# Performance work log

Measured on AMD Instinct MI355X. Metric: run time of the kernel, lower is better.

Reference implementation:

```python
import jax, jax.numpy as jnp
import numpy as np

B, H, S, D = 2, 12, 2048, 64

def setup_inputs() -> dict:
    key = jax.random.key(0)
    kq, kk, kv = jax.random.split(key, 3)
    Q = jax.random.normal(kq, (B, H, S, D), dtype=jnp.float32)
    K = jax.random.normal(kk, (B, H, S, D), dtype=jnp.float32)
    V = jax.random.normal(kv, (B, H, S, D), dtype=jnp.float32)
    return {"Q": Q, "K": K, "V": V}

def reference(Q, K, V):
    # NOTE: original code scales by sqrt(Q.shape[-2]) (the sequence length),
    # not the head dim — reproduced faithfully.
    scale = 1.0 / np.sqrt(Q.shape[-2]).astype(np.float32)
    scores = jnp.einsum('bhqd,bhkd->bhqk', Q, K) * scale  # [B,H,S,S]
    attn = jax.nn.softmax(scores, axis=-1)
    context = jnp.einsum('bhqk,bhkd->bhqd', attn, V)      # [B,H,S,D]
    # torch .squeeze(-1) only removes the last dim if it is size 1; D=64 so no-op
    return context
```

## Files before the change

### kernel.cpp

```cpp
#include <hip/hip_runtime.h>
#include <hip/hip_bf16.h>
#include <math.h>
#include <stdint.h>

#define BATCH 2
#define NH 12
#define SEQ 2048
#define HD 64
#define TQ 64
#define TK 64
#define NHEADS (BATCH*NH)
#define NIT (SEQ / TK)

typedef short bf16x8 __attribute__((ext_vector_type(8)));
typedef float f32x4 __attribute__((ext_vector_type(4)));
typedef float f32x16 __attribute__((ext_vector_type(16)));
typedef unsigned short us4_t __attribute__((ext_vector_type(4)));
typedef unsigned short us8_t __attribute__((ext_vector_type(8)));
typedef unsigned int u32x4 __attribute__((ext_vector_type(4)));

#if __has_builtin(__builtin_amdgcn_exp2f)
#define EXP2F(x) __builtin_amdgcn_exp2f(x)
#else
#define EXP2F(x) exp2f(x)
#endif

static __device__ __forceinline__ unsigned short f2bf(float f) {
    unsigned int u = __float_as_uint(f);
    u += 0x7fffu + ((u >> 16) & 1u);
    return (unsigned short)(u >> 16);
}

static __device__ __forceinline__ unsigned int pack2bf(float a, float b) {
    __hip_bfloat162 v = __float22bfloat162_rn(float2{a, b});
    return *(unsigned int*)&v;
}

static __device__ __forceinline__ void async_cp16(const void* g, void* l) {
    __builtin_amdgcn_global_load_lds(
        (const __attribute__((address_space(1))) void*)g,
        (__attribute__((address_space(3))) void*)(uintptr_t)l,
        16, 0, 0);
}

static __device__ __forceinline__ int tile_off(int r, int c) {
    int rp  = r >> 1;
    int pos = (((r & 1) << 3) | c) ^ (rp & 15);
    return rp * 128 + pos * 8;
}

__global__ __launch_bounds__(256)
void prep_kv(const float* __restrict__ K, const float* __restrict__ V,
             unsigned short* __restrict__ Kb, unsigned short* __restrict__ Vtb) {
    __shared__ unsigned short T[64][66];
    const int bh = blockIdx.x >> 5;
    const int s0 = (blockIdx.x & 31) * 64;
    const int tid = threadIdx.x;
    const size_t off = ((size_t)bh * SEQ + s0) * HD;

    #pragma unroll
    for (int u = 0; u < 4; ++u) {
        int idx = u * 1024 + tid * 4;
        float4 a = *(const float4*)&K[off + idx];
        us4_t r4 = { f2bf(a.x), f2bf(a.y), f2bf(a.z), f2bf(a.w) };
        *(us4_t*)&Kb[off + idx] = r4;
    }
    #pragma unroll
    for (int u = 0; u < 4; ++u) {
        int idx = u * 1024 + tid * 4;
        int r = idx >> 6, col = idx & 63;
        float4 a = *(const float4*)&V[off + idx];
        *(unsigned int*)&T[r][col]     = pack2bf(a.x, a.y);
        *(unsigned int*)&T[r][col + 2] = pack2bf(a.z, a.w);
    }
    __syncthreads();
    unsigned short* Vdst = Vtb + (size_t)bh * HD * SEQ;
    const int g = tid & 7, dd = tid >> 3;
    #pragma unroll
    for (int h = 0; h < 2; ++h) {
        int d = dd + 32 * h;
        us8_t r8;
        #pragma unroll
        for (int j = 0; j < 8; ++j) {
            int src = ((g >> 1) << 4) + ((j >> 2) << 3) + ((g & 1) << 2) + (j & 3);
            r8[j] = T[src][d];
        }
        *(us8_t*)&Vdst[(size_t)d * SEQ + s0 + g * 8] = r8;
    }
}

__global__ __launch_bounds__(256, 4)
void fa_main(const float* __restrict__ Q,
             const unsigned short* __restrict__ Kb,
             const unsigned short* __restrict__ Vtb,
             float* __restrict__ O, float qs) {
    const int x  = blockIdx.x & 7;
    const int t  = blockIdx.x >> 3;
    const int bh = x + 8 * (t % 3);
    const int qt = t / 3;
    const int q0 = qt * TQ;

    __shared__ __align__(16) unsigned char SH[33280];
    unsigned short* Ksh0 = (unsigned short*)SH;
    unsigned short* Ksh1 = (unsigned short*)(SH + 8192);
    unsigned short* Vsh0 = (unsigned short*)(SH + 16384);
    unsigned short* Vsh1 = (unsigned short*)(SH + 24576);
    float* Lsum = (float*)(SH + 32768);
    float* Linv = (float*)(SH + 33024);
    float* ORed = (float*)SH;

    const int tid  = threadIdx.x;
    const int w    = tid >> 6;
    const int mt   = w >> 1;
    const int nt   = w & 1;
    const int lane = tid & 63;
    const int l31  = lane & 31;
    const int hi   = lane >> 5;

    const float*          Qh = Q   + ((size_t)bh * SEQ + q0) * HD;
    const unsigned short* Kh = Kb  + (size_t)bh * SEQ * HD;
    const unsigned short* Vh = Vtb + (size_t)bh * HD * SEQ;

    int rS[2], cS[2];
    #pragma unroll
    for (int i = 0; i < 2; ++i) {
        int rp = w * 8 + 4 * i + (lane >> 4);
        int lc = (lane & 15) ^ (rp & 15);
        rS[i] = 2 * rp + (lc >> 3);
        cS[i] = lc & 7;
    }
    const int dst0 = (w * 8 + 0) * 128, dst1 = (w * 8 + 4) * 128;
    const size_t kG0 = (size_t)rS[0] * HD  + cS[0] * 8;
    const size_t kG1 = (size_t)rS[1] * HD  + cS[1] * 8;
    const size_t vG0 = (size_t)rS[0] * SEQ + cS[0] * 8;
    const size_t vG1 = (size_t)rS[1] * SEQ + cS[1] * 8;

    async_cp16(Kh + kG0, &Ksh0[dst0]);
    async_cp16(Kh + kG1, &Ksh0[dst1]);
    async_cp16(Vh + vG0, &Vsh0[dst0]);
    async_cp16(Vh + vG1, &Vsh0[dst1]);
    #pragma unroll
    for (int u = 0; u < 4; ++u) {
        int idx = u * 1024 + tid * 4;
        int r = idx >> 6, col = idx & 63;
        float4 a = *(const float4*)&Qh[idx];
        uint2 pk = { pack2bf(a.x * qs, a.y * qs), pack2bf(a.z * qs, a.w * qs) };
        *(uint2*)&Vsh1[tile_off(r, col >> 3) + (col & 7)] = pk;
    }
    __syncthreads();

    bf16x8 qf[4];
    #pragma unroll
    for (int s = 0; s < 4; ++s)
        qf[s] = *(const bf16x8*)&Vsh1[tile_off(mt * 32 + l31, s * 2 + hi)];
    __syncthreads();

    int kOffL[4], vOffL[2][2];
    #pragma unroll
    for (int s = 0; s < 4; ++s) kOffL[s] = tile_off(nt * 32 + l31, s * 2 + hi);
    #pragma unroll
    for (int dt = 0; dt < 2; ++dt)
        #pragma unroll
        for (int ks = 0; ks < 2; ++ks)
            vOffL[dt][ks] = tile_off(dt * 32 + l31, nt * 4 + ks * 2 + hi);

    f32x16 o[2];
    o[0] = (f32x16)(0.f);
    o[1] = (f32x16)(0.f);
    float lsum = 0.f;

    #pragma unroll 2
    for (int it = 0; it < NIT; ++it) {
        const int cur = it & 1;
        if (it + 1 < NIT) {
            const size_t kv = (size_t)(it + 1) * TK;
            unsigned short* Kn = cur ? Ksh0 : Ksh1;
            unsigned short* Vn = cur ? Vsh0 : Vsh1;
            async_cp16(Kh + kv * HD + kG0, &Kn[dst0]);
            async_cp16(Kh + kv * HD + kG1, &Kn[dst1]);
            async_cp16(Vh + kv + vG0,      &Vn[dst0]);
            async_cp16(Vh + kv + vG1,      &Vn[dst1]);
        }
        const unsigned short* Ks = cur ? Ksh1 : Ksh0;
        const unsigned short* Vs = cur ? Vsh1 : Vsh0;

        bf16x8 vf[2][2];
        #pragma unroll
        for (int dt = 0; dt < 2; ++dt)
            #pragma unroll
            for (int ks = 0; ks < 2; ++ks)
                vf[dt][ks] = *(const bf16x8*)&Vs[vOffL[dt][ks]];

        f32x16 sc = (f32x16)(0.f);
        #pragma unroll
        for (int s = 0; s < 4; ++s) {
            bf16x8 kf = *(const bf16x8*)&Ks[kOffL[s]];
            sc = __builtin_amdgcn_mfma_f32_32x32x16_bf16(kf, qf[s], sc, 0, 0, 0);
        }

        float e[16];
        #pragma unroll
        for (int r = 0; r < 16; ++r) e[r] = EXP2F(sc[r]);
        #pragma unroll
        for (int r = 0; r < 16; ++r) lsum += e[r];
        union { u32x4 d; bf16x8 h; } pu0, pu1;
        pu0.d = (u32x4){ pack2bf(e[0],  e[1]),  pack2bf(e[2],  e[3]),
                         pack2bf(e[4],  e[5]),  pack2bf(e[6],  e[7]) };
        pu1.d = (u32x4){ pack2bf(e[8],  e[9]),  pack2bf(e[10], e[11]),
                         pack2bf(e[12], e[13]), pack2bf(e[14], e[15]) };
        bf16x8 pf0 = pu0.h, pf1 = pu1.h;

        #pragma unroll
        for (int dt = 0; dt < 2; ++dt) {
            o[dt] = __builtin_amdgcn_mfma_f32_32x32x16_bf16(pf0, vf[dt][0], o[dt], 0, 0, 0);
            o[dt] = __builtin_amdgcn_mfma_f32_32x32x16_bf16(pf1, vf[dt][1], o[dt], 0, 0, 0);
        }

        __syncthreads();
    }

    lsum += __shfl_xor(lsum, 32, 64);

    if (nt == 1) {
        if (lane < 32) Lsum[mt * 32 + lane] = lsum;
        #pragma unroll
        for (int dt = 0; dt < 2; ++dt) {
            const int d = dt * 32 + l31;
            #pragma unroll
            for (int g = 0; g < 4; ++g) {
                const int m0 = mt * 32 + 8 * g + 4 * hi;
                const int ph = (m0 >> 2) ^ (d & 15);
                float4 v = { o[dt][4*g+0], o[dt][4*g+1], o[dt][4*g+2], o[dt][4*g+3] };
                *(float4*)&ORed[d * 64 + ph * 4] = v;
            }
        }
    }
    __syncthreads();

    if (nt == 0) {
        float ltot = lsum + Lsum[mt * 32 + l31];
        if (lane < 32) Linv[mt * 32 + lane] = 1.0f / ltot;
        float* Oh = O + ((size_t)bh * SEQ + q0) * HD;
        #pragma unroll
        for (int dt = 0; dt < 2; ++dt) {
            const int d = dt * 32 + l31;
            #pragma unroll
            for (int g = 0; g < 4; ++g) {
                const int m0 = mt * 32 + 8 * g + 4 * hi;
                const int ph = (m0 >> 2) ^ (d & 15);
                float4 part = *(const float4*)&ORed[d * 64 + ph * 4];
                float4 inv4 = *(const float4*)&Linv[m0];
                const float* pp = (const float*)&part;
                const float* ii = (const float*)&inv4;
                #pragma unroll
                for (int j = 0; j < 4; ++j)
                    Oh[(size_t)(m0 + j) * HD + d] = (o[dt][4*g+j] + pp[j]) * ii[j];
            }
        }
    }
}

#define PAD 8
#define LSTR (HD + PAD)

__global__ __launch_bounds__(256)
void fa_fwd_fb(const float* __restrict__ Q, const float* __restrict__ K,
               const float* __restrict__ V, float* __restrict__ O) {
    const int x  = blockIdx.x & 7;
    const int t  = blockIdx.x >> 3;
    const int bh = x + 8 * (t % 3);
    const int qt = t / 3;
    const int q0 = qt * TQ;
    const long base = (long)bh * SEQ * HD;

    __shared__ unsigned short Qs[TQ][LSTR];
    __shared__ unsigned short Ks2[64][LSTR];
    __shared__ unsigned short Vt[HD][64 + PAD];
    __shared__ unsigned short Ps2[4][16][LSTR];

    const int tid  = threadIdx.x;
    const int wave = tid >> 6;
    const int lane = tid & 63;
    const int col  = lane & 15;
    const int quad = lane >> 4;
    const int m0   = wave * 16;

    #pragma unroll
    for (int i = 0; i < 4; ++i) {
        int idx = tid + 256 * i;
        int row = idx >> 4;
        int c4  = (idx & 15) * 4;
        float4 v = *(const float4*)&Q[base + (long)(q0 + row) * HD + c4];
        ushort4 b = { f2bf(v.x), f2bf(v.y), f2bf(v.z), f2bf(v.w) };
        *(ushort4*)&Qs[row][c4] = b;
    }
    __syncthreads();

    bf16x8 aq0 = *(const bf16x8*)&Qs[m0 + col][quad * 8];
    bf16x8 aq1 = *(const bf16x8*)&Qs[m0 + col][32 + quad * 8];

    f32x4 o0 = {0.f,0.f,0.f,0.f}, o1 = o0, o2 = o0, o3 = o0;
    float l[4] = {0.f, 0.f, 0.f, 0.f};
    const float scale = 0.022097086912079608f;

    for (int kv0 = 0; kv0 < SEQ; kv0 += 64) {
        __syncthreads();
        #pragma unroll
        for (int i = 0; i < 4; ++i) {
            int idx = tid + 256 * i;
            int row = idx >> 4;
            int c4  = (idx & 15) * 4;
            float4 kv = *(const float4*)&K[base + (long)(kv0 + row) * HD + c4];
            ushort4 kb = { f2bf(kv.x), f2bf(kv.y), f2bf(kv.z), f2bf(kv.w) };
            *(ushort4*)&Ks2[row][c4] = kb;
            float4 vv = *(const float4*)&V[base + (long)(kv0 + row) * HD + c4];
            Vt[c4 + 0][row] = f2bf(vv.x);
            Vt[c4 + 1][row] = f2bf(vv.y);
            Vt[c4 + 2][row] = f2bf(vv.z);
            Vt[c4 + 3][row] = f2bf(vv.w);
        }
        __syncthreads();

        f32x4 sc[4];
        #pragma unroll
        for (int n = 0; n < 4; ++n) {
            bf16x8 b0 = *(const bf16x8*)&Ks2[n * 16 + col][quad * 8];
            bf16x8 b1 = *(const bf16x8*)&Ks2[n * 16 + col][32 + quad * 8];
            f32x4 acc = {0.f,0.f,0.f,0.f};
            acc = __builtin_amdgcn_mfma_f32_16x16x32_bf16(aq0, b0, acc, 0, 0, 0);
            acc = __builtin_amdgcn_mfma_f32_16x16x32_bf16(aq1, b1, acc, 0, 0, 0);
            sc[n] = acc;
        }

        float tsum[4] = {0.f, 0.f, 0.f, 0.f};
        #pragma unroll
        for (int n = 0; n < 4; ++n) {
            #pragma unroll
            for (int r = 0; r < 4; ++r) {
                float p = __expf(sc[n][r] * scale);
                tsum[r] += p;
                Ps2[wave][quad * 4 + r][n * 16 + col] = f2bf(p);
            }
        }
        #pragma unroll
        for (int off = 1; off < 16; off <<= 1) {
            #pragma unroll
            for (int r = 0; r < 4; ++r) tsum[r] += __shfl_xor(tsum[r], off, 64);
        }
        #pragma unroll
        for (int r = 0; r < 4; ++r) l[r] += tsum[r];

        bf16x8 ap0 = *(const bf16x8*)&Ps2[wave][col][quad * 8];
        bf16x8 ap1 = *(const bf16x8*)&Ps2[wave][col][32 + quad * 8];
        #pragma unroll
        for (int n = 0; n < 4; ++n) {
            bf16x8 b0 = *(const bf16x8*)&Vt[n * 16 + col][quad * 8];
            bf16x8 b1 = *(const bf16x8*)&Vt[n * 16 + col][32 + quad * 8];
            f32x4* op = (n == 0) ? &o0 : (n == 1) ? &o1 : (n == 2) ? &o2 : &o3;
            *op = __builtin_amdgcn_mfma_f32_16x16x32_bf16(ap0, b0, *op, 0, 0, 0);
            *op = __builtin_amdgcn_mfma_f32_16x16x32_bf16(ap1, b1, *op, 0, 0, 0);
        }
    }

    float inv[4];
    #pragma unroll
    for (int r = 0; r < 4; ++r) inv[r] = 1.0f / l[r];
    #pragma unroll
    for (int r = 0; r < 4; ++r) {
        long row = base + (long)(q0 + m0 + quad * 4 + r) * HD;
        O[row +  0 + col] = o0[r] * inv[r];
        O[row + 16 + col] = o1[r] * inv[r];
        O[row + 32 + col] = o2[r] * inv[r];
        O[row + 48 + col] = o3[r] * inv[r];
    }
}

extern "C" void kernel_launch(void* const* d_in, const int* in_sizes, int n_in,
                              void* d_out, int out_size, void* d_ws, size_t ws_size,
                              hipStream_t stream) {
    const float* Q = (const float*)d_in[0];
    const float* K = (const float*)d_in[1];
    const float* V = (const float*)d_in[2];
    float* O = (float*)d_out;

    const size_t tensorElems = (size_t)NHEADS * SEQ * HD;
    const size_t need = 2 * tensorElems * sizeof(unsigned short);

    if (ws_size >= need) {
        unsigned short* Kb  = (unsigned short*)d_ws;
        unsigned short* Vtb = Kb + tensorElems;
        const float qs = (float)(1.4426950408889634 / sqrt(2048.0));
        prep_kv<<<dim3(NHEADS * (SEQ / 64)), dim3(256), 0, stream>>>(K, V, Kb, Vtb);
        fa_main<<<dim3(NHEADS * (SEQ / TQ)), dim3(256), 0, stream>>>(Q, Kb, Vtb, O, qs);
    } else {
        fa_fwd_fb<<<dim3(NHEADS * (SEQ / TQ)), dim3(256), 0, stream>>>(Q, K, V, O);
    }
}
```

Baseline: 115.7 us.

## Interleave exp and PV MFMA halves with setprio, relax launch bounds

Splits the softmax exponentiation into two halves so the first half's PV MFMAs can issue while the second half's exp2 runs, and wraps the MFMA groups in s_setprio to favour matrix issue across waves. The row-sum is changed to a tree reduction that is done after the MFMAs. The occupancy hint drops from 4 to 3 blocks per CU, which gives the compiler more registers but may leave fewer waves to hide latency.

```diff
diff --git a/kernel.cpp b/kernel.cpp
--- a/kernel.cpp
+++ b/kernel.cpp
@@ -89,7 +89,7 @@
     }
 }
 
-__global__ __launch_bounds__(256, 4)
+__global__ __launch_bounds__(256, 3)
 void fa_main(const float* __restrict__ Q,
              const unsigned short* __restrict__ Kb,
              const unsigned short* __restrict__ Vtb,
@@ -192,29 +192,41 @@
                 vf[dt][ks] = *(const bf16x8*)&Vs[vOffL[dt][ks]];
 
         f32x16 sc = (f32x16)(0.f);
+        __builtin_amdgcn_s_setprio(1);
         #pragma unroll
         for (int s = 0; s < 4; ++s) {
             bf16x8 kf = *(const bf16x8*)&Ks[kOffL[s]];
             sc = __builtin_amdgcn_mfma_f32_32x32x16_bf16(kf, qf[s], sc, 0, 0, 0);
         }
-
-        float e[16];
-        #pragma unroll
-        for (int r = 0; r < 16; ++r) e[r] = EXP2F(sc[r]);
-        #pragma unroll
-        for (int r = 0; r < 16; ++r) lsum += e[r];
+        __builtin_amdgcn_s_setprio(0);
+
+        float e0[8], e1[8];
+        #pragma unroll
+        for (int r = 0; r < 8; ++r) e0[r] = EXP2F(sc[r]);
         union { u32x4 d; bf16x8 h; } pu0, pu1;
-        pu0.d = (u32x4){ pack2bf(e[0],  e[1]),  pack2bf(e[2],  e[3]),
-                         pack2bf(e[4],  e[5]),  pack2bf(e[6],  e[7]) };
-        pu1.d = (u32x4){ pack2bf(e[8],  e[9]),  pack2bf(e[10], e[11]),
-                         pack2bf(e[12], e[13]), pack2bf(e[14], e[15]) };
-        bf16x8 pf0 = pu0.h, pf1 = pu1.h;
-
-        #pragma unroll
-        for (int dt = 0; dt < 2; ++dt) {
-            o[dt] = __builtin_amdgcn_mfma_f32_32x32x16_bf16(pf0, vf[dt][0], o[dt], 0, 0, 0);
-            o[dt] = __builtin_amdgcn_mfma_f32_32x32x16_bf16(pf1, vf[dt][1], o[dt], 0, 0, 0);
-        }
+        pu0.d = (u32x4){ pack2bf(e0[0], e0[1]), pack2bf(e0[2], e0[3]),
+                         pack2bf(e0[4], e0[5]), pack2bf(e0[6], e0[7]) };
+        bf16x8 pf0 = pu0.h;
+        __builtin_amdgcn_s_setprio(1);
+        o[0] = __builtin_amdgcn_mfma_f32_32x32x16_bf16(pf0, vf[0][0], o[0], 0, 0, 0);
+        o[1] = __builtin_amdgcn_mfma_f32_32x32x16_bf16(pf0, vf[1][0], o[1], 0, 0, 0);
+        __builtin_amdgcn_s_setprio(0);
+
+        #pragma unroll
+        for (int r = 0; r < 8; ++r) e1[r] = EXP2F(sc[8 + r]);
+        pu1.d = (u32x4){ pack2bf(e1[0], e1[1]), pack2bf(e1[2], e1[3]),
+                         pack2bf(e1[4], e1[5]), pack2bf(e1[6], e1[7]) };
+        bf16x8 pf1 = pu1.h;
+        __builtin_amdgcn_s_setprio(1);
+        o[0] = __builtin_amdgcn_mfma_f32_32x32x16_bf16(pf1, vf[0][1], o[0], 0, 0, 0);
+        o[1] = __builtin_amdgcn_mfma_f32_32x32x16_bf16(pf1, vf[1][1], o[1], 0, 0, 0);
+        __builtin_amdgcn_s_setprio(0);
+
+        float t0 = ((e0[0] + e0[1]) + (e0[2] + e0[3]))
+                 + ((e0[4] + e0[5]) + (e0[6] + e0[7]));
+        float t1 = ((e1[0] + e1[1]) + (e1[2] + e1[3]))
+                 + ((e1[4] + e1[5]) + (e1[6] + e1[7]));
+        lsum += t0 + t1;
 
         __syncthreads();
     }
```

After: 116.7 us. Within noise of the previous version (+0.9%).
